# Kernel tuning notes

Measured on AMD Instinct MI355X. Metric: run time of the kernel, lower is better.

## Reference

```python
import jax, jax.numpy as jnp
import numpy as np
from jax import lax

B, D, N = 1024, 1024, 65536
M, Ks, DS = 8, 256, 128      # key PQ: subvectors, codewords, subvec dim (D/M)
MV, DV = 8, 256              # value PQ: subvectors, subvec dim (OUT/MV)
OUT = MV * DV
K_TOP = 64


def setup_inputs() -> dict:
    key = jax.random.key(0)
    ks = jax.random.split(key, 7)
    x = jax.random.normal(ks[0], (B, D), dtype=jnp.float32)
    # whitening matrix starts as identity in the module; perturb slightly for a non-trivial test
    whitening_matrix = jnp.eye(D, dtype=jnp.float32) + 0.01 * jax.random.normal(ks[1], (D, D), dtype=jnp.float32)
    key_codebooks = jax.random.normal(ks[2], (M, Ks, DS), dtype=jnp.float32)
    value_codebooks = jax.random.normal(ks[3], (MV, Ks, DV), dtype=jnp.float32)
    bias = jnp.zeros((OUT,), dtype=jnp.float32)
    key_codes = jax.random.randint(ks[4], (N, M), 0, Ks, dtype=jnp.int32)
    value_codes = jax.random.randint(ks[5], (N, MV), 0, Ks, dtype=jnp.int32)
    return {
        "x": x,
        "whitening_matrix": whitening_matrix,
        "key_codebooks": key_codebooks,
        "value_codebooks": value_codebooks,
        "bias": bias,
        "key_codes": key_codes,
        "value_codes": value_codes,
        "k": K_TOP,
    }


def reference(x, whitening_matrix, key_codebooks, value_codebooks, bias, key_codes, value_codes, k):
    # 1) whiten the query (module buffer 'whitening_matrix')
    q = x @ whitening_matrix                      # [B, D]
    qs = q.reshape(B, M, DS)                      # [B, M, DS] query subvectors

    # 2) ADC distance tables: squared L2 between each query subvector and each codeword
    #    dt[b, m, c] = ||qs[b,m] - cb[m,c]||^2
    q_sq = jnp.sum(qs * qs, axis=-1)              # [B, M]
    c_sq = jnp.sum(key_codebooks * key_codebooks, axis=-1)  # [M, Ks]
    cross = jnp.einsum("bmd,mcd->bmc", qs, key_codebooks)   # [B, M, Ks]
    dt = q_sq[:, :, None] + c_sq[None, :, :] - 2.0 * cross  # [B, M, Ks]

    # 3) asymmetric distance to all N stored keys via code gather (irregular access)
    lut = dt.transpose(1, 0, 2)                   # [M, B, Ks]
    # per-subvector gather then sum: d[b, n] = sum_m lut[m, b, key_codes[n, m]]
    dists = jax.vmap(lambda l, c: l[:, c])(lut, key_codes.T).sum(axis=0)  # [B, N]

    # 4) top-k nearest neighbors
    neg_top, top_idx = lax.top_k(-dists, k)       # [B, k]

    # 5) reconstruct values of retrieved neighbors from value PQ codebooks
    vc = value_codes[top_idx]                     # [B, k, MV] int codes
    vals = value_codebooks[jnp.arange(MV)[None, None, :], vc]  # [B, k, MV, DV]
    vals = vals.reshape(vals.shape[0], vals.shape[1], OUT)      # [B, k, OUT]

    # 6) distance-weighted aggregation (softmax over negative distances) + bias
    w = jax.nn.softmax(neg_top, axis=-1)          # [B, k]
    y = jnp.einsum("bk,bko->bo", w, vals) + bias  # [B, OUT]
    return y
```

## Files before the change

kernel.cpp:

```cpp
#include <hip/hip_runtime.h>

#define N_ITEMS 65536

__launch_bounds__(256)
__global__ void gemm_q_kernel(const float* __restrict__ A,
                              const float* __restrict__ W,
                              float* __restrict__ qpart) {
  __shared__ float As[16][132];
  __shared__ float Bs[16][132];
  const int tid = threadIdx.x;
  const int tx = tid & 15, ty = tid >> 4;
  const int rb = blockIdx.y * 128, cb = blockIdx.x * 128;
  const int kz = blockIdx.z * 128;
  const int ar = tid >> 2, ac = (tid & 3) << 2;
  const int bk = tid >> 5, bc = (tid & 31) << 2;

  float4 va0 = *(const float4*)&A[(rb + ar) * 1024 + kz + ac];
  float4 va1 = *(const float4*)&A[(rb + ar + 64) * 1024 + kz + ac];
  float4 vb0 = *(const float4*)&W[(kz + bk) * 1024 + cb + bc];
  float4 vb1 = *(const float4*)&W[(kz + bk + 8) * 1024 + cb + bc];

  float acc[8][8] = {};
  for (int k0 = 0; k0 < 128; k0 += 16) {
    As[ac + 0][ar] = va0.x; As[ac + 1][ar] = va0.y;
    As[ac + 2][ar] = va0.z; As[ac + 3][ar] = va0.w;
    As[ac + 0][ar + 64] = va1.x; As[ac + 1][ar + 64] = va1.y;
    As[ac + 2][ar + 64] = va1.z; As[ac + 3][ar + 64] = va1.w;
    *(float4*)&Bs[bk][bc] = vb0;
    *(float4*)&Bs[bk + 8][bc] = vb1;
    __syncthreads();
    if (k0 + 16 < 128) {
      va0 = *(const float4*)&A[(rb + ar) * 1024 + kz + k0 + 16 + ac];
      va1 = *(const float4*)&A[(rb + ar + 64) * 1024 + kz + k0 + 16 + ac];
      vb0 = *(const float4*)&W[(kz + k0 + 16 + bk) * 1024 + cb + bc];
      vb1 = *(const float4*)&W[(kz + k0 + 16 + bk + 8) * 1024 + cb + bc];
    }
#pragma unroll
    for (int kk = 0; kk < 16; kk++) {
      const float4 a0 = *(const float4*)&As[kk][ty << 2];
      const float4 a1 = *(const float4*)&As[kk][64 + (ty << 2)];
      const float4 b0 = *(const float4*)&Bs[kk][tx << 2];
      const float4 b1 = *(const float4*)&Bs[kk][64 + (tx << 2)];
      const float ar8[8] = {a0.x, a0.y, a0.z, a0.w, a1.x, a1.y, a1.z, a1.w};
      const float br8[8] = {b0.x, b0.y, b0.z, b0.w, b1.x, b1.y, b1.z, b1.w};
#pragma unroll
      for (int r = 0; r < 8; r++)
#pragma unroll
        for (int c = 0; c < 8; c++)
          acc[r][c] = fmaf(ar8[r], br8[c], acc[r][c]);
    }
    __syncthreads();
  }
  float* outp = qpart + blockIdx.z * 1048576;
#pragma unroll
  for (int rh = 0; rh < 2; rh++)
#pragma unroll
    for (int r = 0; r < 4; r++) {
      const int row = rb + rh * 64 + (ty << 2) + r;
      const int ri = rh * 4 + r;
      *(float4*)&outp[row * 1024 + cb + (tx << 2)] =
          make_float4(acc[ri][0], acc[ri][1], acc[ri][2], acc[ri][3]);
      *(float4*)&outp[row * 1024 + cb + 64 + (tx << 2)] =
          make_float4(acc[ri][4], acc[ri][5], acc[ri][6], acc[ri][7]);
    }
}

__launch_bounds__(256)
__global__ void qsum_kernel(const float4* __restrict__ qp,
                            float4* __restrict__ q) {
  const int i = blockIdx.x * 256 + threadIdx.x;
  float4 s0 = qp[i];
  float4 s1 = qp[i + 131072];
#pragma unroll
  for (int z = 1; z < 8; z++) {
    const float4 a = qp[z * 262144 + i];
    const float4 b = qp[z * 262144 + i + 131072];
    s0.x += a.x; s0.y += a.y; s0.z += a.z; s0.w += a.w;
    s1.x += b.x; s1.y += b.y; s1.z += b.z; s1.w += b.w;
  }
  q[i] = s0;
  q[i + 131072] = s1;
}

__launch_bounds__(256)
__global__ void lut_kernel(const float* __restrict__ q,
                           const float* __restrict__ kcb,
                           const int* __restrict__ key_codes,
                           float* __restrict__ lut,
                           unsigned long long* __restrict__ pcodes,
                           uint4* __restrict__ poffs) {
  if (blockIdx.z == 8) {
    const int g0 = (((int)blockIdx.y * 4 + (int)blockIdx.x) * 256 + (int)threadIdx.x) * 4;
#pragma unroll
    for (int t = 0; t < 4; t++) {
      const int gid = g0 + t;
      unsigned long long p = 0ull;
      unsigned h[8];
#pragma unroll
      for (int j = 0; j < 8; j++) {
        const unsigned c = (unsigned)key_codes[gid * 8 + j] & 255u;
        p |= (unsigned long long)c << (8 * j);
        h[j] = c << 6;
      }
      pcodes[gid] = p;
      poffs[gid] = make_uint4(h[0] | (h[1] << 16), h[2] | (h[3] << 16),
                              h[4] | (h[5] << 16), h[6] | (h[7] << 16));
    }
    return;
  }

  __shared__ float As[32][68];
  __shared__ float Bs[32][68];
  const int tid = threadIdx.x;
  const int tx = tid & 15, ty = tid >> 4;
  const int m = blockIdx.z;
  const int rb = blockIdx.y * 64;
  const int cb0 = blockIdx.x * 64;
  float acc[4][4] = {};
  float qa[4] = {}, cs[4] = {};
  for (int k0 = 0; k0 < 128; k0 += 32) {
#pragma unroll
    for (int l = 0; l < 2; l++) {
      const int e = tid + l * 256;
      const int row = e >> 3, c4 = (e & 7) << 2;
      const float4 va = *(const float4*)&q[(rb + row) * 1024 + m * 128 + k0 + c4];
      As[c4 + 0][row] = va.x; As[c4 + 1][row] = va.y;
      As[c4 + 2][row] = va.z; As[c4 + 3][row] = va.w;
      const float4 vb = *(const float4*)&kcb[(m * 256 + cb0 + row) * 128 + k0 + c4];
      Bs[c4 + 0][row] = vb.x; Bs[c4 + 1][row] = vb.y;
      Bs[c4 + 2][row] = vb.z; Bs[c4 + 3][row] = vb.w;
    }
    __syncthreads();
#pragma unroll
    for (int kk = 0; kk < 32; kk++) {
      const float4 a = *(const float4*)&As[kk][ty << 2];
      const float4 b = *(const float4*)&Bs[kk][tx << 2];
      const float ar[4] = {a.x, a.y, a.z, a.w};
      const float br[4] = {b.x, b.y, b.z, b.w};
#pragma unroll
      for (int r = 0; r < 4; r++)
#pragma unroll
        for (int c = 0; c < 4; c++)
          acc[r][c] = fmaf(ar[r], br[c], acc[r][c]);
#pragma unroll
      for (int r = 0; r < 4; r++) qa[r] = fmaf(ar[r], ar[r], qa[r]);
#pragma unroll
      for (int c = 0; c < 4; c++) cs[c] = fmaf(br[c], br[c], cs[c]);
    }
    __syncthreads();
  }
#pragma unroll
  for (int r = 0; r < 4; r++) {
    const int row = rb + (ty << 2) + r;
    const int col = cb0 + (tx << 2);
    float4 v;
    v.x = qa[r] + cs[0] - 2.0f * acc[r][0];
    v.y = qa[r] + cs[1] - 2.0f * acc[r][1];
    v.z = qa[r] + cs[2] - 2.0f * acc[r][2];
    v.w = qa[r] + cs[3] - 2.0f * acc[r][3];
    *(float4*)&lut[row * 2048 + m * 256 + col] = v;
  }
}

extern __shared__ char dyn_lds[];

__launch_bounds__(1024)
__global__ void scansel_kernel(const float* __restrict__ lutf,
                               const uint4* __restrict__ poffs,
                               const unsigned long long* __restrict__ pcodes,
                               const int* __restrict__ value_codes,
                               const float* __restrict__ vcb,
                               const float* __restrict__ bias,
                               float* __restrict__ out) {
  char* repb = dyn_lds;
  unsigned char* temps = (unsigned char*)(dyn_lds + 131072);
  unsigned* tempw = (unsigned*)(dyn_lds + 131072);
  const int tid = threadIdx.x;
  const int g = blockIdx.x;

  {
    const int w = tid >> 6, lane = tid & 63;
#pragma unroll
    for (int t0 = 0; t0 < 2; t0++) {
      const int t = w + t0 * 16;
      const int rr = t & 3, seg = t >> 2;
      const int row = (g << 2) + rr;
      const int e0 = seg * 256 + lane * 4;
      const float4 v4 = *(const float4*)&lutf[row * 2048 + e0];
      float s4 = v4.x + v4.y + v4.z + v4.w;
#pragma unroll
      for (int off = 32; off > 0; off >>= 1) s4 += __shfl_xor(s4, off);
      const float mean = s4 * (1.0f / 256.0f);
      const float vals[4] = {v4.x, v4.y, v4.z, v4.w};
#pragma unroll
      for (int k = 0; k < 4; k++) {
        int iv = (int)rintf(vals[k] - mean);
        iv = max(-127, min(127, iv));
        temps[(e0 + k) * 4 + rr] = (unsigned char)(iv + 128);
      }
    }
  }
  __syncthreads();

  {
    const int lane = tid & 63;
    const unsigned v0 = tempw[tid * 2];
    const unsigned v1 = tempw[tid * 2 + 1];
    const uint4 q0 = make_uint4(v0, v0, v0, v0);
    const uint4 q1 = make_uint4(v1, v1, v1, v1);
    uint4* repv = (uint4*)dyn_lds;
#pragma unroll
    for (int k = 0; k < 4; k++) {
      const int kk = (k + lane) & 3;
      repv[tid * 8 + kk] = q0;
      repv[tid * 8 + 4 + kk] = q1;
    }
  }
  __syncthreads();

  const int r = tid & 15;
  const char* base0 = repb + (r << 2);
  const char* base1 = repb + 65536 + (r << 2);
  unsigned k0[4], k1[4];
#pragma unroll
  for (int j = 0; j < 4; j++) { k0[j] = 0xFFFFFFFFu; k1[j] = 0xFFFFFFFFu; }

  unsigned A[8], B[8];

  auto issue = [&](unsigned (&BUF)[8], const uint4 cw) {
    BUF[0] = *(const unsigned*)(base0 + (cw.x & 0xFFFFu));
    BUF[1] = *(const unsigned*)(base0 + (cw.x >> 16) + 16384);
    BUF[2] = *(const unsigned*)(base0 + (cw.y & 0xFFFFu) + 32768);
    BUF[3] = *(const unsigned*)(base0 + (cw.y >> 16) + 49152);
    BUF[4] = *(const unsigned*)(base1 + (cw.z & 0xFFFFu));
    BUF[5] = *(const unsigned*)(base1 + (cw.z >> 16) + 16384);
    BUF[6] = *(const unsigned*)(base1 + (cw.w & 0xFFFFu) + 32768);
    BUF[7] = *(const unsigned*)(base1 + (cw.w >> 16) + 49152);
  };

  auto consume = [&](const unsigned (&BUF)[8], const int it) {
    const unsigned M = 0x00FF00FFu;
    unsigned accA = BUF[0] & M;
    unsigned accB = (BUF[0] >> 8) & M;
#pragma unroll
    for (int j = 1; j < 8; j++) {
      accA += BUF[j] & M;
      accB += (BUF[j] >> 8) & M;
    }
    const int ss[4] = {(int)(accA & 0xFFFFu), (int)(accB & 0xFFFFu),
                       (int)(accA >> 16), (int)(accB >> 16)};
#pragma unroll
    for (int j = 0; j < 4; j++) {
      const unsigned key = ((unsigned)ss[j] << 6) | (unsigned)it;
      const unsigned mx = (k0[j] > key) ? k0[j] : key;
      k0[j] = (k0[j] < key) ? k0[j] : key;
      k1[j] = (k1[j] < mx) ? k1[j] : mx;
    }
  };

  issue(A, poffs[tid]);
  uint4 cJ1 = poffs[tid + 1024];
  uint4 cJ2 = poffs[tid + 2048];

  for (int it = 0; it < 64; it += 2) {
    const uint4 cN1 = poffs[tid + (((it + 3) & 63) << 10)];
    const uint4 cN2 = poffs[tid + (((it + 4) & 63) << 10)];
    issue(B, cJ1);
    consume(A, it);
    issue(A, cJ2);
    consume(B, it + 1);
    cJ1 = cN1; cJ2 = cN2;
  }

  __syncthreads();

  unsigned* cl  = (unsigned*)dyn_lds;
  float* wts    = (float*)(dyn_lds + 4096);
  unsigned long long* sv8 = (unsigned long long*)(dyn_lds + 8192);
  float* gred   = (float*)(dyn_lds + 16384);
  unsigned* rmin = (unsigned*)(dyn_lds + 16448);
  int* rcnt     = (int*)(dyn_lds + 16464);
  float* rws    = (float*)(dyn_lds + 16480);

  if (tid < 4) { rmin[tid] = 0xFFFFFFFFu; rcnt[tid] = 0; }
  __syncthreads();

#pragma unroll
  for (int j = 0; j < 4; j++) {
    unsigned d = k0[j] >> 6;
#pragma unroll
    for (int off = 32; off > 0; off >>= 1) {
      const unsigned o = __shfl_xor(d, off);
      d = (o < d) ? o : d;
    }
    if ((tid & 63) == 0) atomicMin(&rmin[j], d);
  }
  __syncthreads();

  {
    const int lane = tid & 63;
    const unsigned long long lm = (1ull << lane) - 1ull;
#pragma unroll
    for (int j = 0; j < 4; j++) {
      const unsigned lim = rmin[j] + 20u;
#pragma unroll
      for (int c = 0; c < 2; c++) {
        const unsigned key = c ? k1[j] : k0[j];
        const unsigned d = key >> 6;
        const bool pred = d <= lim;
        const unsigned long long m = __ballot(pred);
        int base = 0;
        if (lane == 0 && m) base = atomicAdd(&rcnt[j], __popcll(m));
        base = __shfl(base, 0);
        if (pred) {
          const int pos = base + __popcll(m & lm);
          if (pos < 256)
            cl[j * 256 + pos] = (d << 16) | ((key & 63u) << 10) | (unsigned)tid;
        }
      }
    }
  }
  __syncthreads();

  const int gj = tid >> 8, gt = tid & 255;
  const int cnt_g = min(rcnt[gj], 256);
  float dex = 1e30f;
  if (gt < cnt_g) {
    const unsigned pc = cl[gj * 256 + gt];
    const int n = (int)(pc & 0xFFFFu);
    const unsigned long long c8 = pcodes[n];
    const uint4 vc0 = *(const uint4*)&value_codes[n * 8];
    const uint4 vc1 = *(const uint4*)&value_codes[n * 8 + 4];
    sv8[gj * 256 + gt] =
        (unsigned long long)(vc0.x & 255u)        | ((unsigned long long)(vc0.y & 255u) << 8)  |
        ((unsigned long long)(vc0.z & 255u) << 16) | ((unsigned long long)(vc0.w & 255u) << 24) |
        ((unsigned long long)(vc1.x & 255u) << 32) | ((unsigned long long)(vc1.y & 255u) << 40) |
        ((unsigned long long)(vc1.z & 255u) << 48) | ((unsigned long long)(vc1.w & 255u) << 56);
    const float* lrow = lutf + ((g << 2) + gj) * 2048;
    const unsigned lo = (unsigned)c8, hi = (unsigned)(c8 >> 32);
    dex  = lrow[        (lo       & 255u)];
    dex += lrow[ 256 + ((lo >>  8) & 255u)];
    dex += lrow[ 512 + ((lo >> 16) & 255u)];
    dex += lrow[ 768 + ((lo >> 24)       )];
    dex += lrow[1024 + ( hi        & 255u)];
    dex += lrow[1280 + ((hi >>  8) & 255u)];
    dex += lrow[1536 + ((hi >> 16) & 255u)];
    dex += lrow[1792 + ((hi >> 24)       )];
  }
  float mnf = dex;
#pragma unroll
  for (int off = 32; off > 0; off >>= 1) mnf = fminf(mnf, __shfl_xor(mnf, off));
  if ((tid & 63) == 0) gred[gj * 4 + ((tid >> 6) & 3)] = mnf;
  __syncthreads();
  const float dminx = fminf(fminf(gred[gj * 4], gred[gj * 4 + 1]),
                            fminf(gred[gj * 4 + 2], gred[gj * 4 + 3]));
  const float w = (gt < cnt_g) ? __expf(dminx - dex) : 0.f;
  wts[gj * 256 + gt] = w;
  float sw_ = w;
#pragma unroll
  for (int off = 32; off > 0; off >>= 1) sw_ += __shfl_xor(sw_, off);
  __syncthreads();
  if ((tid & 63) == 0) gred[gj * 4 + ((tid >> 6) & 3)] = sw_;
  __syncthreads();
  if (gt == 0)
    rws[gj] = 1.0f / (gred[gj * 4] + gred[gj * 4 + 1] + gred[gj * 4 + 2] + gred[gj * 4 + 3]);
  __syncthreads();

  const int h = tid >> 9, u = tid & 511;
  const int col = u << 2;
  const int mv = col >> 8;
  const int co = col & 255;
  const float* vb2 = vcb + mv * 65536 + co;
  const float4 bb = *(const float4*)&bias[col];
#pragma unroll
  for (int jr = 0; jr < 2; jr++) {
    const int j = (jr << 1) | h;
    const int row = (g << 2) + j;
    const int cj = min(rcnt[j], 256);
    float4 acc = make_float4(0.f, 0.f, 0.f, 0.f);
    int k = 0;
    for (; k + 1 < cj; k += 2) {
      const float w0 = wts[j * 256 + k];
      const float w1 = wts[j * 256 + k + 1];
      const unsigned c0 = (unsigned)((sv8[j * 256 + k] >> (mv * 8)) & 255ull);
      const unsigned c1 = (unsigned)((sv8[j * 256 + k + 1] >> (mv * 8)) & 255ull);
      const float4 v0 = *(const float4*)(vb2 + c0 * 256);
      const float4 v1 = *(const float4*)(vb2 + c1 * 256);
      acc.x = fmaf(w0, v0.x, acc.x); acc.y = fmaf(w0, v0.y, acc.y);
      acc.z = fmaf(w0, v0.z, acc.z); acc.w = fmaf(w0, v0.w, acc.w);
      acc.x = fmaf(w1, v1.x, acc.x); acc.y = fmaf(w1, v1.y, acc.y);
      acc.z = fmaf(w1, v1.z, acc.z); acc.w = fmaf(w1, v1.w, acc.w);
    }
    if (k < cj) {
      const float w0 = wts[j * 256 + k];
      const unsigned c0 = (unsigned)((sv8[j * 256 + k] >> (mv * 8)) & 255ull);
      const float4 v0 = *(const float4*)(vb2 + c0 * 256);
      acc.x = fmaf(w0, v0.x, acc.x); acc.y = fmaf(w0, v0.y, acc.y);
      acc.z = fmaf(w0, v0.z, acc.z); acc.w = fmaf(w0, v0.w, acc.w);
    }
    const float iv = rws[j];
    *(float4*)&out[row * 2048 + col] =
        make_float4(fmaf(acc.x, iv, bb.x), fmaf(acc.y, iv, bb.y),
                    fmaf(acc.z, iv, bb.z), fmaf(acc.w, iv, bb.w));
  }
}

__launch_bounds__(512)
__global__ void scan16_kernel(const float* __restrict__ lut,
                              const unsigned long long* __restrict__ pcodes,
                              unsigned* __restrict__ cand_d,
                              unsigned short* __restrict__ cand_n) {
  __shared__ short sRep[32768];
  const int tid = threadIdx.x;
  const int b = blockIdx.x;

  const float4 v4 = *(const float4*)&lut[b * 2048 + tid * 4];
  float s4 = v4.x + v4.y + v4.z + v4.w;
#pragma unroll
  for (int off = 32; off > 0; off >>= 1) s4 += __shfl_xor(s4, off);
  const float mean = s4 * (1.0f / 256.0f);

  const float vals[4] = {v4.x, v4.y, v4.z, v4.w};
#pragma unroll
  for (int k2 = 0; k2 < 4; k2++) {
    float f = (vals[k2] - mean) * 64.0f;
    f = fmaxf(fminf(f, 32000.0f), -32000.0f);
    const int iv = (int)rintf(f);
    const unsigned hw = (unsigned)(unsigned short)iv;
    const unsigned wrd = hw | (hw << 16);
    const uint4 wv = make_uint4(wrd, wrd, wrd, wrd);
    const int e = tid * 4 + k2;
    *(uint4*)&((unsigned*)sRep)[e * 8] = wv;
    *(uint4*)&((unsigned*)sRep)[e * 8 + 4] = wv;
  }
  __syncthreads();

  const int r = tid & 15;
  int d0 = 0x7FFFFFFF, d1 = 0x7FFFFFFF, d2 = 0x7FFFFFFF, d3 = 0x7FFFFFFF;
  int i0 = 0, i1 = 0, i2 = 0, i3 = 0;

  unsigned long long c8 = pcodes[tid];
  for (int it = 0; it < 128; it++) {
    const int n = tid + (it << 9);
    unsigned long long nxt = 0ull;
    if (it < 127) nxt = pcodes[n + 512];
    const unsigned lo = (unsigned)c8;
    const unsigned hi = (unsigned)(c8 >> 32);
    int s;
    s  = sRep[(((lo      ) & 255u) << 4) + r        ];
    s += sRep[(((lo >>  8) & 255u) << 4) + r +  4096];
    s += sRep[(((lo >> 16) & 255u) << 4) + r +  8192];
    s += sRep[(((lo >> 24)       ) << 4) + r + 12288];
    s += sRep[(((hi      ) & 255u) << 4) + r + 16384];
    s += sRep[(((hi >>  8) & 255u) << 4) + r + 20480];
    s += sRep[(((hi >> 16) & 255u) << 4) + r + 24576];
    s += sRep[(((hi >> 24)       ) << 4) + r + 28672];
    if (s < d3) {
      if (s < d1) {
        if (s < d0) { d3 = d2; i3 = i2; d2 = d1; i2 = i1; d1 = d0; i1 = i0; d0 = s; i0 = n; }
        else        { d3 = d2; i3 = i2; d2 = d1; i2 = i1; d1 = s; i1 = n; }
      } else {
        if (s < d2) { d3 = d2; i3 = i2; d2 = s; i2 = n; }
        else        { d3 = s; i3 = n; }
      }
    }
    c8 = nxt;
  }

  const int base = b * 2048 + tid * 4;
  const uint4 dv = make_uint4((unsigned)(d0 + 0x40000000), (unsigned)(d1 + 0x40000000),
                              (unsigned)(d2 + 0x40000000), (unsigned)(d3 + 0x40000000));
  *(uint4*)&cand_d[base] = dv;
  const unsigned ni01 = (unsigned)i0 | ((unsigned)i1 << 16);
  const unsigned ni23 = (unsigned)i2 | ((unsigned)i3 << 16);
  *(uint2*)&cand_n[base] = make_uint2(ni01, ni23);
}

__launch_bounds__(256)
__global__ void select_kernel(const unsigned* __restrict__ cand_d,
                              const unsigned short* __restrict__ cand_n,
                              const int* __restrict__ value_codes,
                              const float* __restrict__ vcb,
                              const float* __restrict__ bias,
                              const unsigned long long* __restrict__ pcodes,
                              const float* __restrict__ lutf,
                              const unsigned lim_add,
                              float* __restrict__ out) {
  __shared__ unsigned sredw[4];
  __shared__ float sredf[4];
  __shared__ unsigned long long clist[256];
  __shared__ float sw[256];
  __shared__ int svc[2048];
  __shared__ int scnt;
  __shared__ float sWsum;

  const int tid = threadIdx.x;
  const int b = blockIdx.x;

  const uint4 a0 = *(const uint4*)&cand_d[b * 2048 + tid * 8];
  const uint4 a1 = *(const uint4*)&cand_d[b * 2048 + tid * 8 + 4];
  const uint4 nn = *(const uint4*)&cand_n[b * 2048 + tid * 8];
  unsigned dk[8] = {a0.x, a0.y, a0.z, a0.w, a1.x, a1.y, a1.z, a1.w};
  unsigned ni[8] = {nn.x & 0xFFFFu, nn.x >> 16, nn.y & 0xFFFFu, nn.y >> 16,
                    nn.z & 0xFFFFu, nn.z >> 16, nn.w & 0xFFFFu, nn.w >> 16};

  if (tid == 0) scnt = 0;
  unsigned mn = dk[0];
#pragma unroll
  for (int j = 1; j < 8; j++) mn = (dk[j] < mn) ? dk[j] : mn;
#pragma unroll
  for (int off = 32; off > 0; off >>= 1) {
    const unsigned o = __shfl_xor(mn, off);
    mn = (o < mn) ? o : mn;
  }
  if ((tid & 63) == 0) sredw[tid >> 6] = mn;
  __syncthreads();
  unsigned sMin = sredw[0];
  sMin = (sredw[1] < sMin) ? sredw[1] : sMin;
  sMin = (sredw[2] < sMin) ? sredw[2] : sMin;
  sMin = (sredw[3] < sMin) ? sredw[3] : sMin;
  const unsigned lim = sMin + lim_add;

  const int lane = tid & 63;
  const unsigned long long lm = (1ull << lane) - 1ull;
#pragma unroll
  for (int j = 0; j < 8; j++) {
    const bool pred = dk[j] <= lim;
    const unsigned long long mask = __ballot(pred);
    int base = 0;
    if (lane == 0 && mask) base = atomicAdd(&scnt, __popcll(mask));
    base = __shfl(base, 0);
    if (pred) {
      const int pos = base + __popcll(mask & lm);
      if (pos < 256) clist[pos] = ((unsigned long long)dk[j] << 32) | ni[j];
    }
  }
  __syncthreads();
  const int cnt = min(scnt, 256);

  float dex = 1e30f;
  if (tid < cnt) {
    const int n = (int)(clist[tid] & 0xFFFFFFFFu);
    const unsigned long long c8 = pcodes[n];
    const float* lrow = lutf + b * 2048;
    const unsigned lo = (unsigned)c8, hi = (unsigned)(c8 >> 32);
    dex  = lrow[        (lo       & 255u)];
    dex += lrow[ 256 + ((lo >>  8) & 255u)];
    dex += lrow[ 512 + ((lo >> 16) & 255u)];
    dex += lrow[ 768 + ((lo >> 24)       )];
    dex += lrow[1024 + ( hi        & 255u)];
    dex += lrow[1280 + ((hi >>  8) & 255u)];
    dex += lrow[1536 + ((hi >> 16) & 255u)];
    dex += lrow[1792 + ((hi >> 24)       )];
  }
  for (int i = tid; i < (cnt << 3); i += 256)
    svc[i] = value_codes[((int)(clist[i >> 3] & 0xFFFFFFFFu)) * 8 + (i & 7)];
  float mnf = dex;
#pragma unroll
  for (int off = 32; off > 0; off >>= 1) mnf = fminf(mnf, __shfl_xor(mnf, off));
  if ((tid & 63) == 0) sredf[tid >> 6] = mnf;
  __syncthreads();
  const float dminx = fminf(fminf(sredf[0], sredf[1]), fminf(sredf[2], sredf[3]));
  if (tid < cnt) sw[tid] = __expf(dminx - dex);
  __syncthreads();

  if (tid < 64) {
    float s = 0.f;
    for (int j = tid; j < cnt; j += 64) s += sw[j];
#pragma unroll
    for (int off = 32; off > 0; off >>= 1) s += __shfl_xor(s, off);
    if (tid == 0) sWsum = s;
  }
  __syncthreads();
  const float inv = 1.0f / sWsum;

  const int c0 = tid << 3;
  const int mv = c0 >> 8;
  const int off = c0 & 255;
  float4 acc0 = make_float4(0.f, 0.f, 0.f, 0.f);
  float4 acc1 = make_float4(0.f, 0.f, 0.f, 0.f);
  const float* vbase = vcb + mv * 65536 + off;
  for (int k = 0; k < cnt; k++) {
    const float w = sw[k];
    const float* vp = vbase + svc[(k << 3) + mv] * 256;
    const float4 v0 = *(const float4*)vp;
    const float4 v1 = *(const float4*)(vp + 4);
    acc0.x = fmaf(w, v0.x, acc0.x); acc0.y = fmaf(w, v0.y, acc0.y);
    acc0.z = fmaf(w, v0.z, acc0.z); acc0.w = fmaf(w, v0.w, acc0.w);
    acc1.x = fmaf(w, v1.x, acc1.x); acc1.y = fmaf(w, v1.y, acc1.y);
    acc1.z = fmaf(w, v1.z, acc1.z); acc1.w = fmaf(w, v1.w, acc1.w);
  }
  const float4 b0 = *(const float4*)&bias[c0];
  const float4 b1 = *(const float4*)&bias[c0 + 4];
  *(float4*)&out[b * 2048 + c0] =
      make_float4(fmaf(acc0.x, inv, b0.x), fmaf(acc0.y, inv, b0.y),
                  fmaf(acc0.z, inv, b0.z), fmaf(acc0.w, inv, b0.w));
  *(float4*)&out[b * 2048 + c0 + 4] =
      make_float4(fmaf(acc1.x, inv, b1.x), fmaf(acc1.y, inv, b1.y),
                  fmaf(acc1.z, inv, b1.z), fmaf(acc1.w, inv, b1.w));
}

extern "C" void kernel_launch(void* const* d_in, const int* in_sizes, int n_in,
                              void* d_out, int out_size, void* d_ws, size_t ws_size,
                              hipStream_t stream) {
  const float* x    = (const float*)d_in[0];
  const float* W    = (const float*)d_in[1];
  const float* kcb  = (const float*)d_in[2];
  const float* vcb  = (const float*)d_in[3];
  const float* bias = (const float*)d_in[4];
  const int* key_codes   = (const int*)d_in[5];
  const int* value_codes = (const int*)d_in[6];
  float* out = (float*)d_out;

  float* qpart = (float*)d_ws;
  float* q     = qpart + 8388608;
  float* lut   = q + 1048576;
  uint4* poffs = (uint4*)(lut + 2097152);
  unsigned long long* pcodes = (unsigned long long*)(poffs + 65536);
  unsigned* cand_d = (unsigned*)d_ws;
  unsigned short* cand_n = (unsigned short*)(cand_d + 2097152);

  hipLaunchKernelGGL(gemm_q_kernel, dim3(8, 8, 8), dim3(256), 0, stream,
                     x, W, qpart);
  hipLaunchKernelGGL(qsum_kernel, dim3(512), dim3(256), 0, stream,
                     (const float4*)qpart, (float4*)q);
  hipLaunchKernelGGL(lut_kernel, dim3(4, 16, 9), dim3(256), 0, stream,
                     q, kcb, key_codes, lut, pcodes, poffs);

  const hipError_t attr_rc = hipFuncSetAttribute(
      (const void*)scansel_kernel, hipFuncAttributeMaxDynamicSharedMemorySize, 139264);
  if (attr_rc == hipSuccess) {
    hipLaunchKernelGGL(scansel_kernel, dim3(256), dim3(1024), 139264, stream,
                       lut, poffs, pcodes, value_codes, vcb, bias, out);
  } else {
    hipLaunchKernelGGL(scan16_kernel, dim3(1024), dim3(512), 0, stream,
                       lut, pcodes, cand_d, cand_n);
    hipLaunchKernelGGL(select_kernel, dim3(1024), dim3(256), 0, stream,
                       cand_d, cand_n, value_codes, vcb, bias, pcodes, lut,
                       1024u, out);
  }
}
```

Measured before the change: 165.8 us.

## Quantize LUT to int8 in lut_kernel and move code packing into GEMM launch

The int8 quantization of the distance table moves out of the scan kernel's prologue and into the LUT GEMM epilogue, which writes a packed 4-row interleaved i8 LUT to global memory. The quantization offset changes from a per-segment mean to the query norm plus a fixed 96. The key-code packing blocks move from the LUT launch into an extra z-slice of the GEMM launch. This removes the scan kernel's reduction, LDS staging pass and one barrier, and lowers its dynamic LDS need, at the cost of an extra global write and read of the i8 LUT. The fixed offset changes quantization accuracy and may affect candidate selection.

```diff
diff --git a/kernel.cpp b/kernel.cpp
--- a/kernel.cpp
+++ b/kernel.cpp
@@ -5,7 +5,30 @@
 __launch_bounds__(256)
 __global__ void gemm_q_kernel(const float* __restrict__ A,
                               const float* __restrict__ W,
-                              float* __restrict__ qpart) {
+                              const int* __restrict__ key_codes,
+                              float* __restrict__ qpart,
+                              unsigned long long* __restrict__ pcodes,
+                              uint4* __restrict__ poffs) {
+  if (blockIdx.z == 8) {
+    const int g0 = (((int)blockIdx.y * 8 + (int)blockIdx.x) * 256 + (int)threadIdx.x) * 4;
+#pragma unroll
+    for (int t = 0; t < 4; t++) {
+      const int gid = g0 + t;
+      unsigned long long p = 0ull;
+      unsigned h[8];
+#pragma unroll
+      for (int j = 0; j < 8; j++) {
+        const unsigned c = (unsigned)key_codes[gid * 8 + j] & 255u;
+        p |= (unsigned long long)c << (8 * j);
+        h[j] = c << 6;
+      }
+      pcodes[gid] = p;
+      poffs[gid] = make_uint4(h[0] | (h[1] << 16), h[2] | (h[3] << 16),
+                              h[4] | (h[5] << 16), h[6] | (h[7] << 16));
+    }
+    return;
+  }
+
   __shared__ float As[16][132];
   __shared__ float Bs[16][132];
   const int tid = threadIdx.x;
@@ -85,30 +108,8 @@
 __launch_bounds__(256)
 __global__ void lut_kernel(const float* __restrict__ q,
                            const float* __restrict__ kcb,
-                           const int* __restrict__ key_codes,
                            float* __restrict__ lut,
-                           unsigned long long* __restrict__ pcodes,
-                           uint4* __restrict__ poffs) {
-  if (blockIdx.z == 8) {
-    const int g0 = (((int)blockIdx.y * 4 + (int)blockIdx.x) * 256 + (int)threadIdx.x) * 4;
-#pragma unroll
-    for (int t = 0; t < 4; t++) {
-      const int gid = g0 + t;
-      unsigned long long p = 0ull;
-      unsigned h[8];
-#pragma unroll
-      for (int j = 0; j < 8; j++) {
-        const unsigned c = (unsigned)key_codes[gid * 8 + j] & 255u;
-        p |= (unsigned long long)c << (8 * j);
-        h[j] = c << 6;
-      }
-      pcodes[gid] = p;
-      poffs[gid] = make_uint4(h[0] | (h[1] << 16), h[2] | (h[3] << 16),
-                              h[4] | (h[5] << 16), h[6] | (h[7] << 16));
-    }
-    return;
-  }
-
+                           unsigned* __restrict__ i8lut) {
   __shared__ float As[32][68];
   __shared__ float Bs[32][68];
   const int tid = threadIdx.x;
@@ -149,6 +150,7 @@
     }
     __syncthreads();
   }
+  unsigned wpk[4] = {0u, 0u, 0u, 0u};
 #pragma unroll
   for (int r = 0; r < 4; r++) {
     const int row = rb + (ty << 2) + r;
@@ -159,13 +161,24 @@
     v.z = qa[r] + cs[2] - 2.0f * acc[r][2];
     v.w = qa[r] + cs[3] - 2.0f * acc[r][3];
     *(float4*)&lut[row * 2048 + m * 256 + col] = v;
-  }
+    const float vb4[4] = {v.x, v.y, v.z, v.w};
+#pragma unroll
+    for (int c = 0; c < 4; c++) {
+      int iv = (int)rintf(vb4[c] - qa[r] - 96.0f);
+      iv = max(-127, min(127, iv));
+      wpk[c] |= (unsigned)(iv + 128) << (8 * r);
+    }
+  }
+  const int gq = (rb >> 2) + ty;
+  const int e0 = m * 256 + cb0 + (tx << 2);
+  *(uint4*)&i8lut[gq * 2048 + e0] = make_uint4(wpk[0], wpk[1], wpk[2], wpk[3]);
 }
 
 extern __shared__ char dyn_lds[];
 
 __launch_bounds__(1024)
 __global__ void scansel_kernel(const float* __restrict__ lutf,
+                               const unsigned* __restrict__ i8lut,
                                const uint4* __restrict__ poffs,
                                const unsigned long long* __restrict__ pcodes,
                                const int* __restrict__ value_codes,
@@ -173,41 +186,14 @@
                                const float* __restrict__ bias,
                                float* __restrict__ out) {
   char* repb = dyn_lds;
-  unsigned char* temps = (unsigned char*)(dyn_lds + 131072);
-  unsigned* tempw = (unsigned*)(dyn_lds + 131072);
   const int tid = threadIdx.x;
   const int g = blockIdx.x;
 
   {
-    const int w = tid >> 6, lane = tid & 63;
-#pragma unroll
-    for (int t0 = 0; t0 < 2; t0++) {
-      const int t = w + t0 * 16;
-      const int rr = t & 3, seg = t >> 2;
-      const int row = (g << 2) + rr;
-      const int e0 = seg * 256 + lane * 4;
-      const float4 v4 = *(const float4*)&lutf[row * 2048 + e0];
-      float s4 = v4.x + v4.y + v4.z + v4.w;
-#pragma unroll
-      for (int off = 32; off > 0; off >>= 1) s4 += __shfl_xor(s4, off);
-      const float mean = s4 * (1.0f / 256.0f);
-      const float vals[4] = {v4.x, v4.y, v4.z, v4.w};
-#pragma unroll
-      for (int k = 0; k < 4; k++) {
-        int iv = (int)rintf(vals[k] - mean);
-        iv = max(-127, min(127, iv));
-        temps[(e0 + k) * 4 + rr] = (unsigned char)(iv + 128);
-      }
-    }
-  }
-  __syncthreads();
-
-  {
     const int lane = tid & 63;
-    const unsigned v0 = tempw[tid * 2];
-    const unsigned v1 = tempw[tid * 2 + 1];
-    const uint4 q0 = make_uint4(v0, v0, v0, v0);
-    const uint4 q1 = make_uint4(v1, v1, v1, v1);
+    const uint2 tv = *(const uint2*)&i8lut[g * 2048 + tid * 2];
+    const uint4 q0 = make_uint4(tv.x, tv.x, tv.x, tv.x);
+    const uint4 q1 = make_uint4(tv.y, tv.y, tv.y, tv.y);
     uint4* repv = (uint4*)dyn_lds;
 #pragma unroll
     for (int k = 0; k < 4; k++) {
@@ -617,21 +603,22 @@
   float* lut   = q + 1048576;
   uint4* poffs = (uint4*)(lut + 2097152);
   unsigned long long* pcodes = (unsigned long long*)(poffs + 65536);
+  unsigned* i8lut = (unsigned*)(pcodes + 65536);
   unsigned* cand_d = (unsigned*)d_ws;
   unsigned short* cand_n = (unsigned short*)(cand_d + 2097152);
 
-  hipLaunchKernelGGL(gemm_q_kernel, dim3(8, 8, 8), dim3(256), 0, stream,
-                     x, W, qpart);
+  hipLaunchKernelGGL(gemm_q_kernel, dim3(8, 8, 9), dim3(256), 0, stream,
+                     x, W, key_codes, qpart, pcodes, poffs);
   hipLaunchKernelGGL(qsum_kernel, dim3(512), dim3(256), 0, stream,
                      (const float4*)qpart, (float4*)q);
-  hipLaunchKernelGGL(lut_kernel, dim3(4, 16, 9), dim3(256), 0, stream,
-                     q, kcb, key_codes, lut, pcodes, poffs);
+  hipLaunchKernelGGL(lut_kernel, dim3(4, 16, 8), dim3(256), 0, stream,
+                     q, kcb, lut, i8lut);
 
   const hipError_t attr_rc = hipFuncSetAttribute(
-      (const void*)scansel_kernel, hipFuncAttributeMaxDynamicSharedMemorySize, 139264);
+      (const void*)scansel_kernel, hipFuncAttributeMaxDynamicSharedMemorySize, 131072);
   if (attr_rc == hipSuccess) {
-    hipLaunchKernelGGL(scansel_kernel, dim3(256), dim3(1024), 139264, stream,
-                       lut, poffs, pcodes, value_codes, vcb, bias, out);
+    hipLaunchKernelGGL(scansel_kernel, dim3(256), dim3(1024), 131072, stream,
+                       lut, i8lut, poffs, pcodes, value_codes, vcb, bias, out);
   } else {
     hipLaunchKernelGGL(scan16_kernel, dim3(1024), dim3(512), 0, stream,
                        lut, pcodes, cand_d, cand_n);
```

Result: no change. 164.3 us, median of 2 (-0.9%).
